# Kernel tuning notes

Measured on AMD Instinct MI355X. Metric: run time of the kernel, lower is better.

The kernel has to match this reference:

```python
import jax, jax.numpy as jnp
import numpy as np

B, N = 32, 1024
CD, GD, HD, OD = 896, 384, 256, 1280  # cluster/geometric/hidden/output dims
EPS_BN = 1e-5


def _w(k, out_d, in_d):
    return jax.random.normal(k, (in_d, out_d), jnp.float32) / np.sqrt(in_d)


def setup_inputs() -> dict:
    key = jax.random.key(0)
    ks = jax.random.split(key, 12)
    return {
        "cluster_features": jax.random.normal(ks[0], (B, N, CD), jnp.float32),
        "geometric_features": jax.random.normal(ks[1], (B, N, GD), jnp.float32),
        "cluster_weights": jax.random.uniform(ks[2], (B, N, N), jnp.float32),
        # linear projections (stored as [in, out])
        "Wq": _w(ks[3], HD, CD), "bq": jnp.zeros((HD,), jnp.float32),
        "Wk": _w(ks[4], HD, GD), "bk": jnp.zeros((HD,), jnp.float32),
        "Wv": _w(ks[5], HD, GD), "bv": jnp.zeros((HD,), jnp.float32),
        "Wcp": _w(ks[6], OD // 2, CD), "bcp": jnp.zeros((OD // 2,), jnp.float32),
        "Wgp": _w(ks[7], OD // 2, HD), "bgp": jnp.zeros((OD // 2,), jnp.float32),
        # fusion head: Linear -> BN(eval) -> ReLU -> (Dropout=identity) -> Linear
        "Wf1": _w(ks[8], OD, OD), "bf1": jnp.zeros((OD,), jnp.float32),
        "bn_gamma": jnp.ones((OD,), jnp.float32),
        "bn_beta": jnp.zeros((OD,), jnp.float32),
        "bn_mean": jnp.zeros((OD,), jnp.float32),
        "bn_var": jnp.ones((OD,), jnp.float32),
        "Wf2": _w(ks[9], OD, OD), "bf2": jnp.zeros((OD,), jnp.float32),
    }


def reference(cluster_features, geometric_features, cluster_weights,
              Wq, bq, Wk, bk, Wv, bv, Wcp, bcp, Wgp, bgp,
              Wf1, bf1, bn_gamma, bn_beta, bn_mean, bn_var, Wf2, bf2):
    Q = cluster_features @ Wq + bq            # [B,N,HD]
    K = geometric_features @ Wk + bk          # [B,N,HD]
    V = geometric_features @ Wv + bv          # [B,N,HD]

    scale = 1.0 / np.sqrt(Q.shape[-1]).astype(np.float32)
    scores = jnp.einsum('bnd,bmd->bnm', Q, K) * scale  # [B,N,N]
    scores = scores + jnp.log(cluster_weights + 1e-8)
    attn = jax.nn.softmax(scores, axis=-1)             # [B,N,N]
    attended = jnp.einsum('bnm,bmd->bnd', attn, V)     # [B,N,HD]

    cluster_pooled = jnp.mean(cluster_features, axis=1)  # [B,CD]
    geom_pooled = jnp.mean(attended, axis=1)             # [B,HD]

    combined = jnp.concatenate([cluster_pooled @ Wcp + bcp,
                                geom_pooled @ Wgp + bgp], axis=-1)  # [B,OD]

    h = combined @ Wf1 + bf1
    h = (h - bn_mean) * jax.lax.rsqrt(bn_var + EPS_BN) * bn_gamma + bn_beta  # BN eval
    h = jax.nn.relu(h)  # dropout is identity at inference
    out = h @ Wf2 + bf2
    return out, attn
```

## Files before the change

### kernel.cpp

```cpp
#include <hip/hip_runtime.h>
#include <stdint.h>

typedef short    v8s  __attribute__((ext_vector_type(8)));
typedef float    v4f  __attribute__((ext_vector_type(4)));
typedef unsigned short u16x8 __attribute__((ext_vector_type(8)));
typedef unsigned short ushort_t;

#define NB   32
#define NN   1024
#define CD   896
#define GD   384
#define HD   256
#define OD   1280
#define SP   1028

static __device__ __forceinline__ unsigned short f2bf(float f) {
    union { float f; unsigned u; } v; v.f = f;
    unsigned r = v.u + 0x7fffu + ((v.u >> 16) & 1u);
    return (unsigned short)(r >> 16);
}

static __device__ __forceinline__ v4f mfma16(v8s a, v8s b, v4f c) {
    return __builtin_amdgcn_mfma_f32_16x16x32_bf16(a, b, c, 0, 0, 0);
}

static __device__ __forceinline__ void stage_cvt16(const float* __restrict__ src, ushort_t* dst) {
    const float4* s4 = (const float4*)src;
    float4 f0 = s4[0], f1 = s4[1], f2 = s4[2], f3 = s4[3];
    u16x8 p0, p1;
    p0[0]=f2bf(f0.x); p0[1]=f2bf(f0.y); p0[2]=f2bf(f0.z); p0[3]=f2bf(f0.w);
    p0[4]=f2bf(f1.x); p0[5]=f2bf(f1.y); p0[6]=f2bf(f1.z); p0[7]=f2bf(f1.w);
    p1[0]=f2bf(f2.x); p1[1]=f2bf(f2.y); p1[2]=f2bf(f2.z); p1[3]=f2bf(f2.w);
    p1[4]=f2bf(f3.x); p1[5]=f2bf(f3.y); p1[6]=f2bf(f3.z); p1[7]=f2bf(f3.w);
    *(u16x8*)dst = p0;
    *(u16x8*)(dst + 8) = p1;
}

static __device__ __forceinline__ void stage_copy16(const ushort_t* __restrict__ src, ushort_t* dst) {
    const u16x8* s = (const u16x8*)src;
    u16x8 a = s[0], b = s[1];
    *(u16x8*)dst = a;
    *(u16x8*)(dst + 8) = b;
}

__global__ void convw_kernel(const float* __restrict__ W, ushort_t* __restrict__ Wt, int Kd) {
    int idx = blockIdx.x * 256 + threadIdx.x;
    int k = idx >> 8, n = idx & 255;
    Wt[(size_t)n * Kd + k] = f2bf(W[idx]);
}

__global__ void zero_kernel(float* __restrict__ p, int n) {
    int i = blockIdx.x * 256 + threadIdx.x;
    if (i < n) p[i] = 0.f;
}

__global__ void pool_kernel(const float* __restrict__ cf, float* __restrict__ pooled) {
    int b = blockIdx.y, chunk = blockIdx.x, t = threadIdx.x;
    if (t >= 224) return;
    const float4* p = (const float4*)(cf + (size_t)(b * NN + chunk * 32) * CD) + t;
    float4 s0{0,0,0,0}, s1{0,0,0,0}, s2{0,0,0,0}, s3{0,0,0,0};
    #pragma unroll 1
    for (int n = 0; n < 32; n += 4) {
        float4 v0 = p[(size_t)(n + 0) * 224];
        float4 v1 = p[(size_t)(n + 1) * 224];
        float4 v2 = p[(size_t)(n + 2) * 224];
        float4 v3 = p[(size_t)(n + 3) * 224];
        s0.x += v0.x; s0.y += v0.y; s0.z += v0.z; s0.w += v0.w;
        s1.x += v1.x; s1.y += v1.y; s1.z += v1.z; s1.w += v1.w;
        s2.x += v2.x; s2.y += v2.y; s2.z += v2.z; s2.w += v2.w;
        s3.x += v3.x; s3.y += v3.y; s3.z += v3.z; s3.w += v3.w;
    }
    const float sc = 1.f / 1024.f;
    float* dst = pooled + b * CD + t * 4;
    atomicAdd(dst + 0, (s0.x + s1.x + s2.x + s3.x) * sc);
    atomicAdd(dst + 1, (s0.y + s1.y + s2.y + s3.y) * sc);
    atomicAdd(dst + 2, (s0.z + s1.z + s2.z + s3.z) * sc);
    atomicAdd(dst + 3, (s0.w + s1.w + s2.w + s3.w) * sc);
}

template<int KD>
__global__ __launch_bounds__(512, 4) void proj_kernel(
    const float* __restrict__ A, const ushort_t* __restrict__ Wt,
    const float* __restrict__ bias, ushort_t* __restrict__ C)
{
    __shared__ ushort_t lA[128 * 40];
    __shared__ ushort_t lB[256 * 40];
    const int tid  = threadIdx.x;
    const int m0   = blockIdx.x * 128;
    const int lane = tid & 63, wave = tid >> 6;
    const int l15  = lane & 15, quad = lane >> 4;
    const int wrow = (wave >> 2) * 64, wcol = (wave & 3) * 64;
    const int srow = tid >> 1, shalf = tid & 1;

    v4f acc[4][4];
    #pragma unroll
    for (int i = 0; i < 4; ++i)
        #pragma unroll
        for (int j = 0; j < 4; ++j) acc[i][j] = v4f{0.f, 0.f, 0.f, 0.f};

    for (int kt = 0; kt < KD / 32; ++kt) {
        if (tid < 256)
            stage_cvt16(A + (size_t)(m0 + srow) * KD + kt * 32 + shalf * 16,
                        &lA[srow * 40 + shalf * 16]);
        stage_copy16(Wt + (size_t)srow * KD + kt * 32 + shalf * 16,
                     &lB[srow * 40 + shalf * 16]);
        __syncthreads();
        v8s af[4], bfr[4];
        #pragma unroll
        for (int rt = 0; rt < 4; ++rt) af[rt]  = *(const v8s*)&lA[(wrow + rt * 16 + l15) * 40 + quad * 8];
        #pragma unroll
        for (int ct = 0; ct < 4; ++ct) bfr[ct] = *(const v8s*)&lB[(wcol + ct * 16 + l15) * 40 + quad * 8];
        #pragma unroll
        for (int rt = 0; rt < 4; ++rt)
            #pragma unroll
            for (int ct = 0; ct < 4; ++ct)
                acc[rt][ct] = mfma16(af[rt], bfr[ct], acc[rt][ct]);
        __syncthreads();
    }

    #pragma unroll
    for (int ct = 0; ct < 4; ++ct) {
        int col = wcol + ct * 16 + l15;
        float bv = bias[col];
        #pragma unroll
        for (int rt = 0; rt < 4; ++rt)
            #pragma unroll
            for (int r = 0; r < 4; ++r) {
                int row = m0 + wrow + rt * 16 + quad * 4 + r;
                C[(size_t)row * 256 + col] = f2bf(acc[rt][ct][r] + bv);
            }
    }
}

__global__ __launch_bounds__(512) void attn_kernel(
    const ushort_t* __restrict__ Qb, const ushort_t* __restrict__ Kb,
    const float* __restrict__ cw,
    float* __restrict__ attn, float* __restrict__ colsum)
{
    __shared__ float S[32 * SP];
    const int bat = blockIdx.x;
    const int m0  = blockIdx.y * 32;
    const int tid = threadIdx.x;
    const int lane = tid & 63, wave = tid >> 6;
    const int l15 = lane & 15, quad = lane >> 4;

    v8s af[2][8];
    #pragma unroll
    for (int rt = 0; rt < 2; ++rt)
        #pragma unroll
        for (int ks = 0; ks < 8; ++ks)
            af[rt][ks] = *(const v8s*)(Qb + (size_t)(bat * NN + m0 + rt * 16 + l15) * HD + ks * 32 + quad * 8);

    const int n0w = wave * 128;
    #pragma unroll 2
    for (int ct = 0; ct < 8; ++ct) {
        const int col = n0w + ct * 16 + l15;
        v8s bfr[8];
        #pragma unroll
        for (int ks = 0; ks < 8; ++ks)
            bfr[ks] = *(const v8s*)(Kb + (size_t)(bat * NN + col) * HD + ks * 32 + quad * 8);
        float w0[4], w1[4];
        const size_t cwb = ((size_t)bat << 20) + col;
        #pragma unroll
        for (int r = 0; r < 4; ++r) {
            w0[r] = cw[cwb + (size_t)(m0 + quad * 4 + r) * NN];
            w1[r] = cw[cwb + (size_t)(m0 + 16 + quad * 4 + r) * NN];
        }
        v4f acc0 = {0.f, 0.f, 0.f, 0.f}, acc1 = {0.f, 0.f, 0.f, 0.f};
        #pragma unroll
        for (int ks = 0; ks < 8; ++ks) {
            acc0 = mfma16(af[0][ks], bfr[ks], acc0);
            acc1 = mfma16(af[1][ks], bfr[ks], acc1);
        }
        #pragma unroll
        for (int r = 0; r < 4; ++r) {
            const int row0 = quad * 4 + r;
            S[row0 * SP + col]        = acc0[r] * 0.0625f + __logf(w0[r] + 1e-8f);
            S[(16 + row0) * SP + col] = acc1[r] * 0.0625f + __logf(w1[r] + 1e-8f);
        }
    }
    __syncthreads();

    float4 cs[4];
    #pragma unroll
    for (int i = 0; i < 4; ++i) cs[i] = float4{0.f, 0.f, 0.f, 0.f};

    #pragma unroll 1
    for (int rr = 0; rr < 4; ++rr) {
        const int row = wave * 4 + rr;
        float* Srow = &S[row * SP];
        float4 v[4];
        #pragma unroll
        for (int i = 0; i < 4; ++i) v[i] = *(float4*)(Srow + i * 256 + lane * 4);
        float m = -1e30f;
        #pragma unroll
        for (int i = 0; i < 4; ++i)
            m = fmaxf(m, fmaxf(fmaxf(v[i].x, v[i].y), fmaxf(v[i].z, v[i].w)));
        #pragma unroll
        for (int off = 1; off <= 32; off <<= 1) m = fmaxf(m, __shfl_xor(m, off));
        float s = 0.f;
        #pragma unroll
        for (int i = 0; i < 4; ++i) {
            v[i].x = __expf(v[i].x - m); v[i].y = __expf(v[i].y - m);
            v[i].z = __expf(v[i].z - m); v[i].w = __expf(v[i].w - m);
            s += v[i].x + v[i].y + v[i].z + v[i].w;
        }
        #pragma unroll
        for (int off = 1; off <= 32; off <<= 1) s += __shfl_xor(s, off);
        const float inv = 1.0f / s;
        float* grow = attn + ((size_t)bat << 20) + (size_t)(m0 + row) * NN;
        #pragma unroll
        for (int i = 0; i < 4; ++i) {
            v[i].x *= inv; v[i].y *= inv; v[i].z *= inv; v[i].w *= inv;
            *(float4*)(grow + i * 256 + lane * 4) = v[i];
            cs[i].x += v[i].x; cs[i].y += v[i].y; cs[i].z += v[i].z; cs[i].w += v[i].w;
        }
    }

    __syncthreads();
    #pragma unroll
    for (int i = 0; i < 4; ++i)
        *(float4*)&S[wave * 1024 + i * 256 + lane * 4] = cs[i];
    __syncthreads();
    {
        const int c = tid * 2;
        float s0 = 0.f, s1 = 0.f;
        #pragma unroll
        for (int w = 0; w < 8; ++w) {
            float2 p = *(const float2*)&S[w * 1024 + c];
            s0 += p.x; s1 += p.y;
        }
        atomicAdd(&colsum[(size_t)bat * NN + c + 0], s0);
        atomicAdd(&colsum[(size_t)bat * NN + c + 1], s1);
    }
}

__global__ __launch_bounds__(192) void wpool_kernel(
    const float* __restrict__ gf, const float* __restrict__ colsum,
    float* __restrict__ gws)
{
    const int b = blockIdx.y, m0 = blockIdx.x * 128, t = threadIdx.x;
    const float2* base = (const float2*)(gf + (size_t)(b * NN + m0) * GD);
    const float* wbase = colsum + (size_t)b * NN + m0;
    float sx = 0.f, sy = 0.f;
    #pragma unroll 4
    for (int m = 0; m < 128; ++m) {
        const float w = wbase[m] * (1.f / 1024.f);
        float2 v = base[(size_t)m * (GD / 2) + t];
        sx += w * v.x; sy += w * v.y;
    }
    atomicAdd(&gws[b * GD + 2 * t + 0], sx);
    atomicAdd(&gws[b * GD + 2 * t + 1], sy);
}

__global__ __launch_bounds__(256) void vproj_kernel(
    const float* __restrict__ gws, const float* __restrict__ Wv,
    const float* __restrict__ bv, float* __restrict__ gpool)
{
    const int b = blockIdx.x, d = threadIdx.x;
    const float* g = gws + (size_t)b * GD;
    float acc = bv[d];
    #pragma unroll 8
    for (int k = 0; k < GD; ++k) acc += g[k] * Wv[(size_t)k * HD + d];
    gpool[b * HD + d] = acc;
}

__global__ void tail1_kernel(const float* __restrict__ pooled, const float* __restrict__ gpool,
                             const float* __restrict__ Wcp, const float* __restrict__ bcp,
                             const float* __restrict__ Wgp, const float* __restrict__ bgp,
                             float* __restrict__ combined)
{
    int idx = blockIdx.x * 256 + threadIdx.x;
    int b = idx / OD, c = idx % OD;
    int kc = blockIdx.y;
    float acc = 0.f;
    if (c < 640) {
        if (kc == 0) acc = bcp[c];
        const float* a = pooled + b * CD;
        const int k0 = kc * 224;
        for (int k = k0; k < k0 + 224; ++k) acc += a[k] * Wcp[k * 640 + c];
    } else {
        int c2 = c - 640;
        if (kc == 0) acc = bgp[c2];
        const float* g = gpool + b * HD;
        const int k0 = kc * 64;
        for (int k = k0; k < k0 + 64; ++k) acc += g[k] * Wgp[k * 640 + c2];
    }
    atomicAdd(&combined[idx], acc);
}

__global__ void tail2_kernel(const float* __restrict__ combined, const float* __restrict__ Wf1,
                             const float* __restrict__ bf1, float* __restrict__ h)
{
    int idx = blockIdx.x * 256 + threadIdx.x;
    int b = idx / OD, c = idx % OD;
    int k0 = blockIdx.y * 256;
    float acc = (blockIdx.y == 0) ? bf1[c] : 0.f;
    const float* a = combined + b * OD;
    for (int k = k0; k < k0 + 256; ++k) acc += a[k] * Wf1[k * OD + c];
    atomicAdd(&h[idx], acc);
}

__global__ void bnrelu_kernel(float* __restrict__ h,
                              const float* __restrict__ g, const float* __restrict__ be,
                              const float* __restrict__ mn, const float* __restrict__ vr)
{
    int idx = blockIdx.x * 256 + threadIdx.x;
    int c = idx % OD;
    float x = (h[idx] - mn[c]) * rsqrtf(vr[c] + 1e-5f) * g[c] + be[c];
    h[idx] = fmaxf(x, 0.f);
}

__global__ void tail3_kernel(const float* __restrict__ h, const float* __restrict__ Wf2,
                             const float* __restrict__ bf2, float* __restrict__ out)
{
    int idx = blockIdx.x * 256 + threadIdx.x;
    int b = idx / OD, c = idx % OD;
    int k0 = blockIdx.y * 256;
    float acc = (blockIdx.y == 0) ? bf2[c] : 0.f;
    const float* a = h + b * OD;
    for (int k = k0; k < k0 + 256; ++k) acc += a[k] * Wf2[k * OD + c];
    atomicAdd(&out[idx], acc);
}

extern "C" void kernel_launch(void* const* d_in, const int* in_sizes, int n_in,
                              void* d_out, int out_size, void* d_ws, size_t ws_size,
                              hipStream_t stream)
{
    const float* cf  = (const float*)d_in[0];
    const float* gf  = (const float*)d_in[1];
    const float* cw  = (const float*)d_in[2];
    const float* Wq  = (const float*)d_in[3];  const float* bq  = (const float*)d_in[4];
    const float* Wk  = (const float*)d_in[5];  const float* bk  = (const float*)d_in[6];
    const float* Wv  = (const float*)d_in[7];  const float* bv  = (const float*)d_in[8];
    const float* Wcp = (const float*)d_in[9];  const float* bcp = (const float*)d_in[10];
    const float* Wgp = (const float*)d_in[11]; const float* bgp = (const float*)d_in[12];
    const float* Wf1 = (const float*)d_in[13]; const float* bf1 = (const float*)d_in[14];
    const float* bng = (const float*)d_in[15]; const float* bnb = (const float*)d_in[16];
    const float* bnm = (const float*)d_in[17]; const float* bnv = (const float*)d_in[18];
    const float* Wf2 = (const float*)d_in[19]; const float* bf2 = (const float*)d_in[20];

    float* out  = (float*)d_out;
    float* attn = out + NB * OD;

    char* w = (char*)d_ws;
    ushort_t* Qb  = (ushort_t*)w; w += (size_t)NB * NN * HD * 2;
    ushort_t* Kb  = (ushort_t*)w; w += (size_t)NB * NN * HD * 2;
    ushort_t* Wqt = (ushort_t*)w; w += (size_t)HD * CD * 2;
    ushort_t* Wkt = (ushort_t*)w; w += (size_t)HD * GD * 2;
    float* pooled   = (float*)w; w += (size_t)NB * CD * 4;
    float* gpool    = (float*)w; w += (size_t)NB * HD * 4;
    float* colsum   = (float*)w; w += (size_t)NB * NN * 4;
    float* gws      = (float*)w; w += (size_t)NB * GD * 4;
    float* combined = (float*)w; w += (size_t)NB * OD * 4;
    float* hbuf     = (float*)w; w += (size_t)NB * OD * 4;

    const int nz = NB * (CD + HD + NN + GD + OD + OD);
    zero_kernel<<<dim3((nz + 255) / 256), dim3(256), 0, stream>>>(pooled, nz);
    zero_kernel<<<dim3((NB * OD + 255) / 256), dim3(256), 0, stream>>>(out, NB * OD);
    convw_kernel<<<dim3(CD), dim3(256), 0, stream>>>(Wq, Wqt, CD);
    convw_kernel<<<dim3(GD), dim3(256), 0, stream>>>(Wk, Wkt, GD);
    pool_kernel<<<dim3(32, 32), dim3(256), 0, stream>>>(cf, pooled);

    proj_kernel<CD><<<dim3(256), dim3(512), 0, stream>>>(cf, Wqt, bq, Qb);
    proj_kernel<GD><<<dim3(256), dim3(512), 0, stream>>>(gf, Wkt, bk, Kb);

    attn_kernel<<<dim3(32, 32), dim3(512), 0, stream>>>(Qb, Kb, cw, attn, colsum);

    wpool_kernel<<<dim3(8, 32), dim3(192), 0, stream>>>(gf, colsum, gws);
    vproj_kernel<<<dim3(32), dim3(256), 0, stream>>>(gws, Wv, bv, gpool);

    tail1_kernel<<<dim3(160, 4), dim3(256), 0, stream>>>(pooled, gpool, Wcp, bcp, Wgp, bgp, combined);
    tail2_kernel<<<dim3(160, 5), dim3(256), 0, stream>>>(combined, Wf1, bf1, hbuf);
    bnrelu_kernel<<<dim3(160), dim3(256), 0, stream>>>(hbuf, bng, bnb, bnm, bnv);
    tail3_kernel<<<dim3(160, 5), dim3(256), 0, stream>>>(hbuf, Wf2, bf2, out);
}
```

Before: 690.4 us.

## Double-buffer projection GEMM, merge weight conversion, fuse BN into final linear

The projection GEMM now double-buffers its LDS tiles and prefetches the next K-slice into registers while the MFMAs run. The launch-bounds occupancy hint is dropped, and LDS use per block doubles. The two weight-conversion kernels become one launch, and the attention kernel is split into two launches of 16 batches each. BN+ReLU is fused into tail3, which now runs the full K loop per thread without atomics, so the output zeroing launch is gone but each thread does more serial work.

```diff
diff --git a/kernel.cpp b/kernel.cpp
--- a/kernel.cpp
+++ b/kernel.cpp
@@ -24,29 +24,43 @@
     return __builtin_amdgcn_mfma_f32_16x16x32_bf16(a, b, c, 0, 0, 0);
 }
 
-static __device__ __forceinline__ void stage_cvt16(const float* __restrict__ src, ushort_t* dst) {
+struct ARegs { float4 f[4]; };
+struct BRegs { u16x8 h[2]; };
+
+static __device__ __forceinline__ void load_a(ARegs& r, const float* __restrict__ src) {
     const float4* s4 = (const float4*)src;
-    float4 f0 = s4[0], f1 = s4[1], f2 = s4[2], f3 = s4[3];
+    r.f[0] = s4[0]; r.f[1] = s4[1]; r.f[2] = s4[2]; r.f[3] = s4[3];
+}
+static __device__ __forceinline__ void store_a(ushort_t* dst, const ARegs& r) {
     u16x8 p0, p1;
-    p0[0]=f2bf(f0.x); p0[1]=f2bf(f0.y); p0[2]=f2bf(f0.z); p0[3]=f2bf(f0.w);
-    p0[4]=f2bf(f1.x); p0[5]=f2bf(f1.y); p0[6]=f2bf(f1.z); p0[7]=f2bf(f1.w);
-    p1[0]=f2bf(f2.x); p1[1]=f2bf(f2.y); p1[2]=f2bf(f2.z); p1[3]=f2bf(f2.w);
-    p1[4]=f2bf(f3.x); p1[5]=f2bf(f3.y); p1[6]=f2bf(f3.z); p1[7]=f2bf(f3.w);
+    p0[0]=f2bf(r.f[0].x); p0[1]=f2bf(r.f[0].y); p0[2]=f2bf(r.f[0].z); p0[3]=f2bf(r.f[0].w);
+    p0[4]=f2bf(r.f[1].x); p0[5]=f2bf(r.f[1].y); p0[6]=f2bf(r.f[1].z); p0[7]=f2bf(r.f[1].w);
+    p1[0]=f2bf(r.f[2].x); p1[1]=f2bf(r.f[2].y); p1[2]=f2bf(r.f[2].z); p1[3]=f2bf(r.f[2].w);
+    p1[4]=f2bf(r.f[3].x); p1[5]=f2bf(r.f[3].y); p1[6]=f2bf(r.f[3].z); p1[7]=f2bf(r.f[3].w);
     *(u16x8*)dst = p0;
     *(u16x8*)(dst + 8) = p1;
 }
-
-static __device__ __forceinline__ void stage_copy16(const ushort_t* __restrict__ src, ushort_t* dst) {
+static __device__ __forceinline__ void load_b(BRegs& r, const ushort_t* __restrict__ src) {
     const u16x8* s = (const u16x8*)src;
-    u16x8 a = s[0], b = s[1];
-    *(u16x8*)dst = a;
-    *(u16x8*)(dst + 8) = b;
-}
-
-__global__ void convw_kernel(const float* __restrict__ W, ushort_t* __restrict__ Wt, int Kd) {
-    int idx = blockIdx.x * 256 + threadIdx.x;
-    int k = idx >> 8, n = idx & 255;
-    Wt[(size_t)n * Kd + k] = f2bf(W[idx]);
+    r.h[0] = s[0]; r.h[1] = s[1];
+}
+static __device__ __forceinline__ void store_b(ushort_t* dst, const BRegs& r) {
+    *(u16x8*)dst = r.h[0];
+    *(u16x8*)(dst + 8) = r.h[1];
+}
+
+__global__ void convw2_kernel(const float* __restrict__ Wq, ushort_t* __restrict__ Wqt,
+                              const float* __restrict__ Wk, ushort_t* __restrict__ Wkt) {
+    int bx = blockIdx.x;
+    if (bx < CD) {
+        int idx = bx * 256 + threadIdx.x;
+        int k = idx >> 8, n = idx & 255;
+        Wqt[(size_t)n * CD + k] = f2bf(Wq[idx]);
+    } else {
+        int idx = (bx - CD) * 256 + threadIdx.x;
+        int k = idx >> 8, n = idx & 255;
+        Wkt[(size_t)n * GD + k] = f2bf(Wk[idx]);
+    }
 }
 
 __global__ void zero_kernel(float* __restrict__ p, int n) {
@@ -79,18 +93,19 @@
 }
 
 template<int KD>
-__global__ __launch_bounds__(512, 4) void proj_kernel(
+__global__ __launch_bounds__(512) void proj_kernel(
     const float* __restrict__ A, const ushort_t* __restrict__ Wt,
     const float* __restrict__ bias, ushort_t* __restrict__ C)
 {
-    __shared__ ushort_t lA[128 * 40];
-    __shared__ ushort_t lB[256 * 40];
+    __shared__ ushort_t lA[2][128 * 40];
+    __shared__ ushort_t lB[2][256 * 40];
     const int tid  = threadIdx.x;
     const int m0   = blockIdx.x * 128;
     const int lane = tid & 63, wave = tid >> 6;
     const int l15  = lane & 15, quad = lane >> 4;
     const int wrow = (wave >> 2) * 64, wcol = (wave & 3) * 64;
     const int srow = tid >> 1, shalf = tid & 1;
+    const int KT   = KD / 32;
 
     v4f acc[4][4];
     #pragma unroll
@@ -98,23 +113,38 @@
         #pragma unroll
         for (int j = 0; j < 4; ++j) acc[i][j] = v4f{0.f, 0.f, 0.f, 0.f};
 
-    for (int kt = 0; kt < KD / 32; ++kt) {
-        if (tid < 256)
-            stage_cvt16(A + (size_t)(m0 + srow) * KD + kt * 32 + shalf * 16,
-                        &lA[srow * 40 + shalf * 16]);
-        stage_copy16(Wt + (size_t)srow * KD + kt * 32 + shalf * 16,
-                     &lB[srow * 40 + shalf * 16]);
-        __syncthreads();
+    ARegs ar; BRegs br;
+    if (tid < 256) {
+        load_a(ar, A + (size_t)(m0 + srow) * KD + shalf * 16);
+        store_a(&lA[0][srow * 40 + shalf * 16], ar);
+    }
+    load_b(br, Wt + (size_t)srow * KD + shalf * 16);
+    store_b(&lB[0][srow * 40 + shalf * 16], br);
+    __syncthreads();
+
+    for (int kt = 0; kt < KT; ++kt) {
+        const int p = kt & 1;
+        if (kt + 1 < KT) {
+            if (tid < 256)
+                load_a(ar, A + (size_t)(m0 + srow) * KD + (kt + 1) * 32 + shalf * 16);
+            load_b(br, Wt + (size_t)srow * KD + (kt + 1) * 32 + shalf * 16);
+        }
         v8s af[4], bfr[4];
         #pragma unroll
-        for (int rt = 0; rt < 4; ++rt) af[rt]  = *(const v8s*)&lA[(wrow + rt * 16 + l15) * 40 + quad * 8];
-        #pragma unroll
-        for (int ct = 0; ct < 4; ++ct) bfr[ct] = *(const v8s*)&lB[(wcol + ct * 16 + l15) * 40 + quad * 8];
+        for (int rt = 0; rt < 4; ++rt) af[rt]  = *(const v8s*)&lA[p][(wrow + rt * 16 + l15) * 40 + quad * 8];
+        #pragma unroll
+        for (int ct = 0; ct < 4; ++ct) bfr[ct] = *(const v8s*)&lB[p][(wcol + ct * 16 + l15) * 40 + quad * 8];
         #pragma unroll
         for (int rt = 0; rt < 4; ++rt)
             #pragma unroll
             for (int ct = 0; ct < 4; ++ct)
                 acc[rt][ct] = mfma16(af[rt], bfr[ct], acc[rt][ct]);
+        __syncthreads();
+        if (kt + 1 < KT) {
+            if (tid < 256)
+                store_a(&lA[p ^ 1][srow * 40 + shalf * 16], ar);
+            store_b(&lB[p ^ 1][srow * 40 + shalf * 16], br);
+        }
         __syncthreads();
     }
 
@@ -135,10 +165,10 @@
 __global__ __launch_bounds__(512) void attn_kernel(
     const ushort_t* __restrict__ Qb, const ushort_t* __restrict__ Kb,
     const float* __restrict__ cw,
-    float* __restrict__ attn, float* __restrict__ colsum)
+    float* __restrict__ attn, float* __restrict__ colsum, int bat0)
 {
     __shared__ float S[32 * SP];
-    const int bat = blockIdx.x;
+    const int bat = bat0 + blockIdx.x;
     const int m0  = blockIdx.y * 32;
     const int tid = threadIdx.x;
     const int lane = tid & 63, wave = tid >> 6;
@@ -301,26 +331,33 @@
     atomicAdd(&h[idx], acc);
 }
 
-__global__ void bnrelu_kernel(float* __restrict__ h,
-                              const float* __restrict__ g, const float* __restrict__ be,
-                              const float* __restrict__ mn, const float* __restrict__ vr)
-{
-    int idx = blockIdx.x * 256 + threadIdx.x;
-    int c = idx % OD;
-    float x = (h[idx] - mn[c]) * rsqrtf(vr[c] + 1e-5f) * g[c] + be[c];
-    h[idx] = fmaxf(x, 0.f);
-}
-
 __global__ void tail3_kernel(const float* __restrict__ h, const float* __restrict__ Wf2,
-                             const float* __restrict__ bf2, float* __restrict__ out)
+                             const float* __restrict__ bf2,
+                             const float* __restrict__ g, const float* __restrict__ be,
+                             const float* __restrict__ mn, const float* __restrict__ vr,
+                             float* __restrict__ out)
 {
     int idx = blockIdx.x * 256 + threadIdx.x;
     int b = idx / OD, c = idx % OD;
-    int k0 = blockIdx.y * 256;
-    float acc = (blockIdx.y == 0) ? bf2[c] : 0.f;
     const float* a = h + b * OD;
-    for (int k = k0; k < k0 + 256; ++k) acc += a[k] * Wf2[k * OD + c];
-    atomicAdd(&out[idx], acc);
+    float a0 = 0.f, a1 = 0.f, a2 = 0.f, a3 = 0.f;
+    #pragma unroll 1
+    for (int k = 0; k < OD; k += 4) {
+        float4 av = *(const float4*)(a + k);
+        float s0 = rsqrtf(vr[k + 0] + 1e-5f) * g[k + 0];
+        float s1 = rsqrtf(vr[k + 1] + 1e-5f) * g[k + 1];
+        float s2 = rsqrtf(vr[k + 2] + 1e-5f) * g[k + 2];
+        float s3 = rsqrtf(vr[k + 3] + 1e-5f) * g[k + 3];
+        float x0 = fmaxf((av.x - mn[k + 0]) * s0 + be[k + 0], 0.f);
+        float x1 = fmaxf((av.y - mn[k + 1]) * s1 + be[k + 1], 0.f);
+        float x2 = fmaxf((av.z - mn[k + 2]) * s2 + be[k + 2], 0.f);
+        float x3 = fmaxf((av.w - mn[k + 3]) * s3 + be[k + 3], 0.f);
+        a0 += x0 * Wf2[(size_t)(k + 0) * OD + c];
+        a1 += x1 * Wf2[(size_t)(k + 1) * OD + c];
+        a2 += x2 * Wf2[(size_t)(k + 2) * OD + c];
+        a3 += x3 * Wf2[(size_t)(k + 3) * OD + c];
+    }
+    out[idx] = bf2[c] + (a0 + a1) + (a2 + a3);
 }
 
 extern "C" void kernel_launch(void* const* d_in, const int* in_sizes, int n_in,
@@ -357,21 +394,19 @@
 
     const int nz = NB * (CD + HD + NN + GD + OD + OD);
     zero_kernel<<<dim3((nz + 255) / 256), dim3(256), 0, stream>>>(pooled, nz);
-    zero_kernel<<<dim3((NB * OD + 255) / 256), dim3(256), 0, stream>>>(out, NB * OD);
-    convw_kernel<<<dim3(CD), dim3(256), 0, stream>>>(Wq, Wqt, CD);
-    convw_kernel<<<dim3(GD), dim3(256), 0, stream>>>(Wk, Wkt, GD);
+    convw2_kernel<<<dim3(CD + GD), dim3(256), 0, stream>>>(Wq, Wqt, Wk, Wkt);
     pool_kernel<<<dim3(32, 32), dim3(256), 0, stream>>>(cf, pooled);
 
     proj_kernel<CD><<<dim3(256), dim3(512), 0, stream>>>(cf, Wqt, bq, Qb);
     proj_kernel<GD><<<dim3(256), dim3(512), 0, stream>>>(gf, Wkt, bk, Kb);
 
-    attn_kernel<<<dim3(32, 32), dim3(512), 0, stream>>>(Qb, Kb, cw, attn, colsum);
+    attn_kernel<<<dim3(16, 32), dim3(512), 0, stream>>>(Qb, Kb, cw, attn, colsum, 0);
+    attn_kernel<<<dim3(16, 32), dim3(512), 0, stream>>>(Qb, Kb, cw, attn, colsum, 16);
 
     wpool_kernel<<<dim3(8, 32), dim3(192), 0, stream>>>(gf, colsum, gws);
     vproj_kernel<<<dim3(32), dim3(256), 0, stream>>>(gws, Wv, bv, gpool);
 
     tail1_kernel<<<dim3(160, 4), dim3(256), 0, stream>>>(pooled, gpool, Wcp, bcp, Wgp, bgp, combined);
     tail2_kernel<<<dim3(160, 5), dim3(256), 0, stream>>>(combined, Wf1, bf1, hbuf);
-    bnrelu_kernel<<<dim3(160), dim3(256), 0, stream>>>(hbuf, bng, bnb, bnm, bnv);
-    tail3_kernel<<<dim3(160, 5), dim3(256), 0, stream>>>(hbuf, Wf2, bf2, out);
-}
+    tail3_kernel<<<dim3(160), dim3(256), 0, stream>>>(hbuf, Wf2, bf2, bng, bnb, bnm, bnv, out);
+}
```

After: 831.4 us. +20.4%, slower.
